# Performance work log

Hardware: AMD Instinct MI355X
Metric: run time of the kernel (lower is better)

Reference implementation:

```python
import jax, jax.numpy as jnp
import numpy as np

N_NODES = 100000
N_EDGES = 1600000


def _tconv(x, src, dst, Wq, bq, Wk, bk, Wv, bv, Ws, bs):
    """PyG TransformerConv (heads=1, concat=True, root_weight=True), eval mode."""
    n = x.shape[0]
    q = x @ Wq + bq          # [N, d]
    k = x @ Wk + bk
    v = x @ Wv + bv
    scale = 1.0 / jnp.sqrt(jnp.asarray(q.shape[1], q.dtype))
    # per-edge attention logits: query at destination, key at source
    alpha = jnp.sum(q[dst] * k[src], axis=-1) * scale       # [E]
    # segment softmax over incoming edges of each destination node
    m = jax.ops.segment_max(alpha, dst, num_segments=n)      # [N]
    e = jnp.exp(alpha - m[dst])
    s = jax.ops.segment_sum(e, dst, num_segments=n)          # [N]
    a = e / s[dst]                                           # [E]
    agg = jax.ops.segment_sum(a[:, None] * v[src], dst, num_segments=n)  # [N, d]
    return agg + x @ Ws + bs  # skip connection (root_weight=True)


def setup_inputs() -> dict:
    key = jax.random.key(0)
    ks = jax.random.split(key, 20)
    x = jax.random.normal(ks[0], (N_NODES, 2), dtype=jnp.float32)
    edge_index = jax.random.randint(ks[1], (2, N_EDGES), 0, N_NODES, dtype=jnp.int64)
    def lin(k, din, dout):
        k1, k2 = jax.random.split(k)
        lim = 1.0 / np.sqrt(din)
        W = jax.random.uniform(k1, (din, dout), jnp.float32, -lim, lim)
        b = jax.random.uniform(k2, (dout,), jnp.float32, -lim, lim)
        return W, b
    Wq1, bq1 = lin(ks[2], 2, 256)
    Wk1, bk1 = lin(ks[3], 2, 256)
    Wv1, bv1 = lin(ks[4], 2, 256)
    Ws1, bs1 = lin(ks[5], 2, 256)
    Wq2, bq2 = lin(ks[6], 256, 2)
    Wk2, bk2 = lin(ks[7], 256, 2)
    Wv2, bv2 = lin(ks[8], 256, 2)
    Ws2, bs2 = lin(ks[9], 256, 2)
    return dict(x=x, edge_index=edge_index,
                Wq1=Wq1, bq1=bq1, Wk1=Wk1, bk1=bk1, Wv1=Wv1, bv1=bv1, Ws1=Ws1, bs1=bs1,
                Wq2=Wq2, bq2=bq2, Wk2=Wk2, bk2=bk2, Wv2=Wv2, bv2=bv2, Ws2=Ws2, bs2=bs2)


def reference(x, edge_index,
              Wq1, bq1, Wk1, bk1, Wv1, bv1, Ws1, bs1,
              Wq2, bq2, Wk2, bk2, Wv2, bv2, Ws2, bs2):
    src, dst = edge_index[0], edge_index[1]
    h = _tconv(x, src, dst, Wq1, bq1, Wk1, bk1, Wv1, bv1, Ws1, bs1)
    h = jax.nn.relu(h)
    # F.dropout is identity in eval mode
    h = _tconv(h, src, dst, Wq2, bq2, Wk2, bk2, Wv2, bv2, Ws2, bs2)
    return jax.nn.log_softmax(h, axis=1)
```

## Files before the change

kernel.cpp:

```cpp
#include <hip/hip_runtime.h>


#define R_LOG2   7
#define R_DSTS   128
#define BE       4096
#define MAXNB    1024
#define CAPB     2432
#define RSQRT2   0.70710678118654752f

__global__ __launch_bounds__(1024) void scatter1_k(
        const int* __restrict__ src, const int* __restrict__ dst,
        int* __restrict__ cnt, int* __restrict__ recs, int NB, int E) {
    __shared__ int hist[MAXNB];
    __shared__ int lofs[MAXNB];
    __shared__ int gbase[MAXNB];
    __shared__ int stage[BE];
    __shared__ unsigned short sbkt[BE];
    __shared__ int wsum[16];
    int t = threadIdx.x;
    if (t < NB) hist[t] = 0;
    __syncthreads();

    int base = blockIdx.x * BE;
    int nloc = E - base; if (nloc > BE) nloc = BE;
    int nv = nloc >> 2;
    const int4* d4 = (const int4*)(dst + base);
    const int4* s4 = (const int4*)(src + base);

    for (int i = t; i < nv; i += 1024) {
        int4 v = d4[i];
        atomicAdd(&hist[v.x >> R_LOG2], 1);
        atomicAdd(&hist[v.y >> R_LOG2], 1);
        atomicAdd(&hist[v.z >> R_LOG2], 1);
        atomicAdd(&hist[v.w >> R_LOG2], 1);
    }
    for (int i = (nv << 2) + t; i < nloc; i += 1024)
        atomicAdd(&hist[dst[base + i] >> R_LOG2], 1);
    __syncthreads();

    {
        int v = (t < NB) ? hist[t] : 0;
        int lane = t & 63, w = t >> 6;
        int incl = v;
#pragma unroll
        for (int o = 1; o < 64; o <<= 1) {
            int u = __shfl_up(incl, o);
            if (lane >= o) incl += u;
        }
        if (lane == 63) wsum[w] = incl;
        __syncthreads();
        int ex = incl - v;
        for (int j = 0; j < w; ++j) ex += wsum[j];
        if (t < NB) lofs[t] = ex;
    }
    __syncthreads();

    if (t < NB) {
        int h = hist[t];
        int start = h ? atomicAdd(&cnt[t], h) : 0;
        gbase[t] = t * CAPB + start - lofs[t];
        hist[t] = 0;
    }
    __syncthreads();

    for (int i = t; i < nv; i += 1024) {
        int4 dv = d4[i];
        int4 sv = s4[i];
        int d, b, r, p;
        d = dv.x; b = d >> R_LOG2; r = atomicAdd(&hist[b], 1); p = lofs[b] + r;
        stage[p] = sv.x | ((d & (R_DSTS - 1)) << 17); sbkt[p] = (unsigned short)b;
        d = dv.y; b = d >> R_LOG2; r = atomicAdd(&hist[b], 1); p = lofs[b] + r;
        stage[p] = sv.y | ((d & (R_DSTS - 1)) << 17); sbkt[p] = (unsigned short)b;
        d = dv.z; b = d >> R_LOG2; r = atomicAdd(&hist[b], 1); p = lofs[b] + r;
        stage[p] = sv.z | ((d & (R_DSTS - 1)) << 17); sbkt[p] = (unsigned short)b;
        d = dv.w; b = d >> R_LOG2; r = atomicAdd(&hist[b], 1); p = lofs[b] + r;
        stage[p] = sv.w | ((d & (R_DSTS - 1)) << 17); sbkt[p] = (unsigned short)b;
    }
    for (int i = (nv << 2) + t; i < nloc; i += 1024) {
        int d = dst[base + i];
        int b = d >> R_LOG2;
        int r = atomicAdd(&hist[b], 1);
        int p = lofs[b] + r;
        stage[p] = src[base + i] | ((d & (R_DSTS - 1)) << 17);
        sbkt[p] = (unsigned short)b;
    }
    __syncthreads();

    for (int i = t; i < nloc; i += 1024) {
        int bk = sbkt[i];
        int p = gbase[bk] + i;
        if (p < (bk + 1) * CAPB) recs[p] = stage[i];
    }
}

__global__ __launch_bounds__(512) void l1agg_k(
        const float* __restrict__ x,
        const float* __restrict__ Wq1, const float* __restrict__ bq1,
        const float* __restrict__ Wk1, const float* __restrict__ bk1,
        const int* __restrict__ recs, const int* __restrict__ cnt,
        float4* __restrict__ agg1, int N) {
    __shared__ float cpart[4][9];
    __shared__ float c9[9];
    __shared__ float p0[R_DSTS], p1[R_DSTS], pc[R_DSTS];
    __shared__ float ac[3 * R_DSTS];
    int t = threadIdx.x;

    if (t < 256) {
        float wq0 = Wq1[t], wq1 = Wq1[256 + t];
        float wk0 = Wk1[t], wk1 = Wk1[256 + t];
        float bq = bq1[t], bk = bk1[t];
        float vals[9] = { wq0 * wk0, wq0 * wk1, wq1 * wk0, wq1 * wk1,
                          wq0 * bk,  wq1 * bk,  bq * wk0,  bq * wk1,  bq * bk };
        int lane = t & 63, w = t >> 6;
#pragma unroll
        for (int i = 0; i < 9; ++i) {
            float v = vals[i];
#pragma unroll
            for (int o = 32; o > 0; o >>= 1) v += __shfl_xor(v, o);
            if (lane == 0) cpart[w][i] = v;
        }
    }
    __syncthreads();
    if (t < 9) c9[t] = cpart[0][t] + cpart[1][t] + cpart[2][t] + cpart[3][t];
    __syncthreads();

    int b = blockIdx.x;
    int nbase = b << R_LOG2;
    int rem = N - nbase; if (rem > R_DSTS) rem = R_DSTS;

    if (t < 3 * R_DSTS) ac[t] = 0.f;
    if (t < rem) {
        float2 xd = ((const float2*)x)[nbase + t];
        p0[t] = c9[0] * xd.x + c9[2] * xd.y + c9[6];
        p1[t] = c9[1] * xd.x + c9[3] * xd.y + c9[7];
        pc[t] = c9[4] * xd.x + c9[5] * xd.y + c9[8];
    }
    __syncthreads();

    int cb = cnt[b]; if (cb > CAPB) cb = CAPB;
    const int* rb = recs + (size_t)b * CAPB;
    for (int i = t; i < cb; i += 512) {
        int rec = rb[i];
        int s = rec & 0x1FFFF;
        int dl = (rec >> 17) & (R_DSTS - 1);
        float2 xs = ((const float2*)x)[s];
        float w = __expf((p0[dl] * xs.x + p1[dl] * xs.y + pc[dl]) * 0.0625f);
        atomicAdd(&ac[dl], w);
        atomicAdd(&ac[R_DSTS + dl], w * xs.x);
        atomicAdd(&ac[2 * R_DSTS + dl], w * xs.y);
    }
    __syncthreads();

    if (t < rem)
        agg1[nbase + t] = make_float4(ac[t], ac[R_DSTS + t], ac[2 * R_DSTS + t], 0.f);
}

__global__ __launch_bounds__(256, 4) void proj_k(
        const float* __restrict__ x, const float4* __restrict__ agg1,
        const float* __restrict__ Wv1, const float* __restrict__ bv1,
        const float* __restrict__ Ws1, const float* __restrict__ bs1,
        const float* __restrict__ Wq2, const float* __restrict__ bq2,
        const float* __restrict__ Wk2, const float* __restrict__ bk2,
        const float* __restrict__ Wv2, const float* __restrict__ bv2,
        const float* __restrict__ Ws2, const float* __restrict__ bs2,
        float* __restrict__ q2, float4* __restrict__ kv2,
        float* __restrict__ hs2, int N) {
    __shared__ float sW[14][256];
    int t = threadIdx.x;
    sW[0][t]  = Wv1[t];
    sW[1][t]  = Wv1[256 + t];
    sW[2][t]  = Ws1[t];
    sW[3][t]  = Ws1[256 + t];
    sW[4][t]  = bv1[t];
    sW[5][t]  = bs1[t];
    sW[6][t]  = Wq2[2 * t];
    sW[7][t]  = Wq2[2 * t + 1];
    sW[8][t]  = Wk2[2 * t];
    sW[9][t]  = Wk2[2 * t + 1];
    sW[10][t] = Wv2[2 * t];
    sW[11][t] = Wv2[2 * t + 1];
    sW[12][t] = Ws2[2 * t];
    sW[13][t] = Ws2[2 * t + 1];
    __syncthreads();

    int g = t & 7;
    int grp = t >> 3;
    int nb = blockIdx.x * 64 + grp * 2;

    float a0[2], a1[2], he[2], xdx[2], xdy[2];
#pragma unroll
    for (int k = 0; k < 2; ++k) {
        int n = nb + k;
        a0[k] = 0.f; a1[k] = 0.f; he[k] = 0.f; xdx[k] = 0.f; xdy[k] = 0.f;
        if (n < N) {
            float4 ag = agg1[n];
            if (ag.x > 0.f) {
                float inv = 1.0f / ag.x;
                a0[k] = ag.y * inv; a1[k] = ag.z * inv; he[k] = 1.f;
            }
            float2 xd = ((const float2*)x)[n];
            xdx[k] = xd.x; xdy[k] = xd.y;
        }
    }

    float acc[2][8];
#pragma unroll
    for (int k = 0; k < 2; ++k)
#pragma unroll
        for (int i = 0; i < 8; ++i) acc[k][i] = 0.f;

#pragma unroll 1
    for (int j = 0; j < 8; ++j) {
        int ci = g + 8 * j;
        float4 hk[2];
        {
            float4 w0 = ((const float4*)sW[0])[ci];
            float4 w1 = ((const float4*)sW[1])[ci];
            float4 w2 = ((const float4*)sW[2])[ci];
            float4 w3 = ((const float4*)sW[3])[ci];
            float4 w4 = ((const float4*)sW[4])[ci];
            float4 w5 = ((const float4*)sW[5])[ci];
#pragma unroll
            for (int k = 0; k < 2; ++k) {
                hk[k].x = fmaxf(a0[k]*w0.x + a1[k]*w1.x + xdx[k]*w2.x + xdy[k]*w3.x + he[k]*w4.x + w5.x, 0.f);
                hk[k].y = fmaxf(a0[k]*w0.y + a1[k]*w1.y + xdx[k]*w2.y + xdy[k]*w3.y + he[k]*w4.y + w5.y, 0.f);
                hk[k].z = fmaxf(a0[k]*w0.z + a1[k]*w1.z + xdx[k]*w2.z + xdy[k]*w3.z + he[k]*w4.z + w5.z, 0.f);
                hk[k].w = fmaxf(a0[k]*w0.w + a1[k]*w1.w + xdx[k]*w2.w + xdy[k]*w3.w + he[k]*w4.w + w5.w, 0.f);
            }
        }
#pragma unroll
        for (int i = 0; i < 8; ++i) {
            float4 u = ((const float4*)sW[6 + i])[ci];
#pragma unroll
            for (int k = 0; k < 2; ++k)
                acc[k][i] += hk[k].x*u.x + hk[k].y*u.y + hk[k].z*u.z + hk[k].w*u.w;
        }
    }
#pragma unroll
    for (int k = 0; k < 2; ++k)
#pragma unroll
        for (int i = 0; i < 8; ++i) {
#pragma unroll
            for (int m = 1; m < 8; m <<= 1)
                acc[k][i] += __shfl_xor(acc[k][i], m);
        }
    if (g < 2) {
        int n = nb + g;
        if (n < N) {
            ((float2*)q2)[n]  = make_float2(acc[g][0] + bq2[0], acc[g][1] + bq2[1]);
            kv2[n] = make_float4(acc[g][2] + bk2[0], acc[g][3] + bk2[1],
                                 acc[g][4] + bv2[0], acc[g][5] + bv2[1]);
            ((float2*)hs2)[n] = make_float2(acc[g][6] + bs2[0], acc[g][7] + bs2[1]);
        }
    }
}

__global__ __launch_bounds__(512) void l2out_k(
        const float* __restrict__ q2, const float4* __restrict__ kv2,
        const float* __restrict__ hs2,
        const int* __restrict__ recs, const int* __restrict__ cnt,
        float* __restrict__ out, int N) {
    __shared__ float qx[R_DSTS], qy[R_DSTS];
    __shared__ float ac[3 * R_DSTS];
    int t = threadIdx.x;
    int b = blockIdx.x;
    int nbase = b << R_LOG2;
    int rem = N - nbase; if (rem > R_DSTS) rem = R_DSTS;

    if (t < 3 * R_DSTS) ac[t] = 0.f;
    if (t < rem) {
        float2 q = ((const float2*)q2)[nbase + t];
        qx[t] = q.x * RSQRT2;
        qy[t] = q.y * RSQRT2;
    }
    __syncthreads();

    int cb = cnt[b]; if (cb > CAPB) cb = CAPB;
    const int* rb = recs + (size_t)b * CAPB;
    for (int i = t; i < cb; i += 512) {
        int rec = rb[i];
        int s = rec & 0x1FFFF;
        int dl = (rec >> 17) & (R_DSTS - 1);
        float4 kv = kv2[s];
        float w = __expf(qx[dl] * kv.x + qy[dl] * kv.y);
        atomicAdd(&ac[dl], w);
        atomicAdd(&ac[R_DSTS + dl], w * kv.z);
        atomicAdd(&ac[2 * R_DSTS + dl], w * kv.w);
    }
    __syncthreads();

    if (t < rem) {
        int n = nbase + t;
        float s = ac[t];
        float g0 = 0.f, g1 = 0.f;
        if (s > 0.f) {
            float inv = 1.0f / s;
            g0 = ac[R_DSTS + t] * inv; g1 = ac[2 * R_DSTS + t] * inv;
        }
        float2 hs = ((const float2*)hs2)[n];
        float o0 = g0 + hs.x;
        float o1 = g1 + hs.y;
        float mx = fmaxf(o0, o1), mn = fminf(o0, o1);
        float lse = mx + log1pf(__expf(mn - mx));
        ((float2*)out)[n] = make_float2(o0 - lse, o1 - lse);
    }
}

extern "C" void kernel_launch(void* const* d_in, const int* in_sizes, int n_in,
                              void* d_out, int out_size, void* d_ws, size_t ws_size,
                              hipStream_t stream) {
    const float* x   = (const float*)d_in[0];
    const int*   ei  = (const int*)d_in[1];
    const float* Wq1 = (const float*)d_in[2];
    const float* bq1 = (const float*)d_in[3];
    const float* Wk1 = (const float*)d_in[4];
    const float* bk1 = (const float*)d_in[5];
    const float* Wv1 = (const float*)d_in[6];
    const float* bv1 = (const float*)d_in[7];
    const float* Ws1 = (const float*)d_in[8];
    const float* bs1 = (const float*)d_in[9];
    const float* Wq2 = (const float*)d_in[10];
    const float* bq2 = (const float*)d_in[11];
    const float* Wk2 = (const float*)d_in[12];
    const float* bk2 = (const float*)d_in[13];
    const float* Wv2 = (const float*)d_in[14];
    const float* bv2 = (const float*)d_in[15];
    const float* Ws2 = (const float*)d_in[16];
    const float* bs2 = (const float*)d_in[17];

    const int N = in_sizes[0] / 2;
    const int E = in_sizes[1] / 2;
    const int* src = ei;
    const int* dst = ei + E;

    const int NB   = (N + R_DSTS - 1) >> R_LOG2;
    const int NBlk = (E + BE - 1) / BE;

    float* ws = (float*)d_ws;
    size_t off = 0;
    int*   cnt   = (int*)(ws + off);         off += NB;
    int*   recs  = (int*)(ws + off);         off += (size_t)NB * CAPB;
    off = (off + 3) & ~(size_t)3;
    float4* agg1 = (float4*)(ws + off);      off += 4 * (size_t)N;
    float4* kv2  = (float4*)(ws + off);      off += 4 * (size_t)N;
    float* q2    = ws + off;                 off += 2 * (size_t)N;
    float* hs2   = ws + off;                 off += 2 * (size_t)N;

    const int gP = (N + 63) / 64;

    hipMemsetAsync(cnt, 0, NB * sizeof(int), stream);
    scatter1_k<<<NBlk, 1024, 0, stream>>>(src, dst, cnt, recs, NB, E);
    l1agg_k<<<NB, 512, 0, stream>>>(x, Wq1, bq1, Wk1, bk1, recs, cnt, agg1, N);
    proj_k<<<gP, 256, 0, stream>>>(x, agg1, Wv1, bv1, Ws1, bs1,
                                   Wq2, bq2, Wk2, bk2, Wv2, bv2, Ws2, bs2,
                                   q2, kv2, hs2, N);
    l2out_k<<<NB, 512, 0, stream>>>(q2, kv2, hs2, recs, cnt, (float*)d_out, N);
}
```

Baseline: 123.3 us.

## Fuse layer-1 aggregation with projection kernel and vectorize edge record loads

Merges the layer-1 attention aggregation kernel with the dense projection kernel, so each 128-destination block projects its own nodes directly from shared-memory accumulators. This removes the agg1 round trip through global memory and one kernel launch. It also reads edge records as int4 in both aggregation loops, so four gathers are in flight per thread. In exchange the fused kernel uses more shared memory (about 14 KB of weights) and runs the projection with 512 threads covering 128 nodes, which may reduce occupancy.

```diff
diff --git a/kernel.cpp b/kernel.cpp
--- a/kernel.cpp
+++ b/kernel.cpp
@@ -93,16 +93,24 @@
     }
 }
 
-__global__ __launch_bounds__(512) void l1agg_k(
+__global__ __launch_bounds__(512) void l1proj_k(
         const float* __restrict__ x,
         const float* __restrict__ Wq1, const float* __restrict__ bq1,
         const float* __restrict__ Wk1, const float* __restrict__ bk1,
+        const float* __restrict__ Wv1, const float* __restrict__ bv1,
+        const float* __restrict__ Ws1, const float* __restrict__ bs1,
+        const float* __restrict__ Wq2, const float* __restrict__ bq2,
+        const float* __restrict__ Wk2, const float* __restrict__ bk2,
+        const float* __restrict__ Wv2, const float* __restrict__ bv2,
+        const float* __restrict__ Ws2, const float* __restrict__ bs2,
         const int* __restrict__ recs, const int* __restrict__ cnt,
-        float4* __restrict__ agg1, int N) {
+        float* __restrict__ q2, float4* __restrict__ kv2,
+        float* __restrict__ hs2, int N) {
     __shared__ float cpart[4][9];
     __shared__ float c9[9];
     __shared__ float p0[R_DSTS], p1[R_DSTS], pc[R_DSTS];
     __shared__ float ac[3 * R_DSTS];
+    __shared__ float sW[14][256];
     int t = threadIdx.x;
 
     if (t < 256) {
@@ -119,8 +127,26 @@
             for (int o = 32; o > 0; o >>= 1) v += __shfl_xor(v, o);
             if (lane == 0) cpart[w][i] = v;
         }
-    }
-    __syncthreads();
+    } else if (t < 512) {
+        int c = t - 256;
+        sW[0][c]  = Wv1[c];
+        sW[1][c]  = Wv1[256 + c];
+        sW[2][c]  = Ws1[c];
+        sW[3][c]  = Ws1[256 + c];
+        sW[4][c]  = bv1[c];
+        sW[5][c]  = bs1[c];
+        sW[6][c]  = Wq2[2 * c];
+        sW[7][c]  = Wq2[2 * c + 1];
+        sW[8][c]  = Wk2[2 * c];
+        sW[9][c]  = Wk2[2 * c + 1];
+        sW[10][c] = Wv2[2 * c];
+        sW[11][c] = Wv2[2 * c + 1];
+        sW[12][c] = Ws2[2 * c];
+        sW[13][c] = Ws2[2 * c + 1];
+    }
+    __syncthreads();
+    if (t < 256) {
+    }
     if (t < 9) c9[t] = cpart[0][t] + cpart[1][t] + cpart[2][t] + cpart[3][t];
     __syncthreads();
 
@@ -137,13 +163,35 @@
     }
     __syncthreads();
 
+    const float2* x2 = (const float2*)x;
     int cb = cnt[b]; if (cb > CAPB) cb = CAPB;
     const int* rb = recs + (size_t)b * CAPB;
-    for (int i = t; i < cb; i += 512) {
+    const int4* rb4 = (const int4*)rb;
+    int nv4 = cb >> 2;
+    for (int i = t; i < nv4; i += 512) {
+        int4 r = rb4[i];
+        int s0 = r.x & 0x1FFFF, d0 = (r.x >> 17) & (R_DSTS - 1);
+        int s1 = r.y & 0x1FFFF, d1 = (r.y >> 17) & (R_DSTS - 1);
+        int s2 = r.z & 0x1FFFF, d2 = (r.z >> 17) & (R_DSTS - 1);
+        int s3 = r.w & 0x1FFFF, d3 = (r.w >> 17) & (R_DSTS - 1);
+        float2 xa = x2[s0];
+        float2 xb = x2[s1];
+        float2 xc = x2[s2];
+        float2 xd = x2[s3];
+        float w0 = __expf((p0[d0] * xa.x + p1[d0] * xa.y + pc[d0]) * 0.0625f);
+        float w1 = __expf((p0[d1] * xb.x + p1[d1] * xb.y + pc[d1]) * 0.0625f);
+        float w2 = __expf((p0[d2] * xc.x + p1[d2] * xc.y + pc[d2]) * 0.0625f);
+        float w3 = __expf((p0[d3] * xd.x + p1[d3] * xd.y + pc[d3]) * 0.0625f);
+        atomicAdd(&ac[d0], w0); atomicAdd(&ac[R_DSTS + d0], w0 * xa.x); atomicAdd(&ac[2 * R_DSTS + d0], w0 * xa.y);
+        atomicAdd(&ac[d1], w1); atomicAdd(&ac[R_DSTS + d1], w1 * xb.x); atomicAdd(&ac[2 * R_DSTS + d1], w1 * xb.y);
+        atomicAdd(&ac[d2], w2); atomicAdd(&ac[R_DSTS + d2], w2 * xc.x); atomicAdd(&ac[2 * R_DSTS + d2], w2 * xc.y);
+        atomicAdd(&ac[d3], w3); atomicAdd(&ac[R_DSTS + d3], w3 * xd.x); atomicAdd(&ac[2 * R_DSTS + d3], w3 * xd.y);
+    }
+    for (int i = (nv4 << 2) + t; i < cb; i += 512) {
         int rec = rb[i];
         int s = rec & 0x1FFFF;
         int dl = (rec >> 17) & (R_DSTS - 1);
-        float2 xs = ((const float2*)x)[s];
+        float2 xs = x2[s];
         float w = __expf((p0[dl] * xs.x + p1[dl] * xs.y + pc[dl]) * 0.0625f);
         atomicAdd(&ac[dl], w);
         atomicAdd(&ac[R_DSTS + dl], w * xs.x);
@@ -151,52 +199,23 @@
     }
     __syncthreads();
 
-    if (t < rem)
-        agg1[nbase + t] = make_float4(ac[t], ac[R_DSTS + t], ac[2 * R_DSTS + t], 0.f);
-}
-
-__global__ __launch_bounds__(256, 4) void proj_k(
-        const float* __restrict__ x, const float4* __restrict__ agg1,
-        const float* __restrict__ Wv1, const float* __restrict__ bv1,
-        const float* __restrict__ Ws1, const float* __restrict__ bs1,
-        const float* __restrict__ Wq2, const float* __restrict__ bq2,
-        const float* __restrict__ Wk2, const float* __restrict__ bk2,
-        const float* __restrict__ Wv2, const float* __restrict__ bv2,
-        const float* __restrict__ Ws2, const float* __restrict__ bs2,
-        float* __restrict__ q2, float4* __restrict__ kv2,
-        float* __restrict__ hs2, int N) {
-    __shared__ float sW[14][256];
-    int t = threadIdx.x;
-    sW[0][t]  = Wv1[t];
-    sW[1][t]  = Wv1[256 + t];
-    sW[2][t]  = Ws1[t];
-    sW[3][t]  = Ws1[256 + t];
-    sW[4][t]  = bv1[t];
-    sW[5][t]  = bs1[t];
-    sW[6][t]  = Wq2[2 * t];
-    sW[7][t]  = Wq2[2 * t + 1];
-    sW[8][t]  = Wk2[2 * t];
-    sW[9][t]  = Wk2[2 * t + 1];
-    sW[10][t] = Wv2[2 * t];
-    sW[11][t] = Wv2[2 * t + 1];
-    sW[12][t] = Ws2[2 * t];
-    sW[13][t] = Ws2[2 * t + 1];
-    __syncthreads();
-
     int g = t & 7;
     int grp = t >> 3;
-    int nb = blockIdx.x * 64 + grp * 2;
+    int i0 = grp * 2;
 
     float a0[2], a1[2], he[2], xdx[2], xdy[2];
 #pragma unroll
     for (int k = 0; k < 2; ++k) {
-        int n = nb + k;
+        int idx = i0 + k;
+        int n = nbase + idx;
         a0[k] = 0.f; a1[k] = 0.f; he[k] = 0.f; xdx[k] = 0.f; xdy[k] = 0.f;
-        if (n < N) {
-            float4 ag = agg1[n];
-            if (ag.x > 0.f) {
-                float inv = 1.0f / ag.x;
-                a0[k] = ag.y * inv; a1[k] = ag.z * inv; he[k] = 1.f;
+        if (idx < rem) {
+            float s = ac[idx];
+            if (s > 0.f) {
+                float inv = 1.0f / s;
+                a0[k] = ac[R_DSTS + idx] * inv;
+                a1[k] = ac[2 * R_DSTS + idx] * inv;
+                he[k] = 1.f;
             }
             float2 xd = ((const float2*)x)[n];
             xdx[k] = xd.x; xdy[k] = xd.y;
@@ -245,8 +264,9 @@
                 acc[k][i] += __shfl_xor(acc[k][i], m);
         }
     if (g < 2) {
-        int n = nb + g;
-        if (n < N) {
+        int idx = i0 + g;
+        int n = nbase + idx;
+        if (idx < rem) {
             ((float2*)q2)[n]  = make_float2(acc[g][0] + bq2[0], acc[g][1] + bq2[1]);
             kv2[n] = make_float4(acc[g][2] + bk2[0], acc[g][3] + bk2[1],
                                  acc[g][4] + bv2[0], acc[g][5] + bv2[1]);
@@ -277,7 +297,28 @@
 
     int cb = cnt[b]; if (cb > CAPB) cb = CAPB;
     const int* rb = recs + (size_t)b * CAPB;
-    for (int i = t; i < cb; i += 512) {
+    const int4* rb4 = (const int4*)rb;
+    int nv4 = cb >> 2;
+    for (int i = t; i < nv4; i += 512) {
+        int4 r = rb4[i];
+        int s0 = r.x & 0x1FFFF, d0 = (r.x >> 17) & (R_DSTS - 1);
+        int s1 = r.y & 0x1FFFF, d1 = (r.y >> 17) & (R_DSTS - 1);
+        int s2 = r.z & 0x1FFFF, d2 = (r.z >> 17) & (R_DSTS - 1);
+        int s3 = r.w & 0x1FFFF, d3 = (r.w >> 17) & (R_DSTS - 1);
+        float4 ka = kv2[s0];
+        float4 kb = kv2[s1];
+        float4 kc = kv2[s2];
+        float4 kd = kv2[s3];
+        float w0 = __expf(qx[d0] * ka.x + qy[d0] * ka.y);
+        float w1 = __expf(qx[d1] * kb.x + qy[d1] * kb.y);
+        float w2 = __expf(qx[d2] * kc.x + qy[d2] * kc.y);
+        float w3 = __expf(qx[d3] * kd.x + qy[d3] * kd.y);
+        atomicAdd(&ac[d0], w0); atomicAdd(&ac[R_DSTS + d0], w0 * ka.z); atomicAdd(&ac[2 * R_DSTS + d0], w0 * ka.w);
+        atomicAdd(&ac[d1], w1); atomicAdd(&ac[R_DSTS + d1], w1 * kb.z); atomicAdd(&ac[2 * R_DSTS + d1], w1 * kb.w);
+        atomicAdd(&ac[d2], w2); atomicAdd(&ac[R_DSTS + d2], w2 * kc.z); atomicAdd(&ac[2 * R_DSTS + d2], w2 * kc.w);
+        atomicAdd(&ac[d3], w3); atomicAdd(&ac[R_DSTS + d3], w3 * kd.z); atomicAdd(&ac[2 * R_DSTS + d3], w3 * kd.w);
+    }
+    for (int i = (nv4 << 2) + t; i < cb; i += 512) {
         int rec = rb[i];
         int s = rec & 0x1FFFF;
         int dl = (rec >> 17) & (R_DSTS - 1);
@@ -338,21 +379,18 @@
 
     float* ws = (float*)d_ws;
     size_t off = 0;
-    int*   cnt   = (int*)(ws + off);         off += NB;
-    int*   recs  = (int*)(ws + off);         off += (size_t)NB * CAPB;
+    int*   cnt  = (int*)(ws + off);      off += MAXNB;
+    int*   recs = (int*)(ws + off);      off += (size_t)NB * CAPB;
     off = (off + 3) & ~(size_t)3;
-    float4* agg1 = (float4*)(ws + off);      off += 4 * (size_t)N;
-    float4* kv2  = (float4*)(ws + off);      off += 4 * (size_t)N;
-    float* q2    = ws + off;                 off += 2 * (size_t)N;
-    float* hs2   = ws + off;                 off += 2 * (size_t)N;
-
-    const int gP = (N + 63) / 64;
+    float4* kv2 = (float4*)(ws + off);   off += 4 * (size_t)N;
+    float* q2   = ws + off;              off += 2 * (size_t)N;
+    float* hs2  = ws + off;              off += 2 * (size_t)N;
 
     hipMemsetAsync(cnt, 0, NB * sizeof(int), stream);
     scatter1_k<<<NBlk, 1024, 0, stream>>>(src, dst, cnt, recs, NB, E);
-    l1agg_k<<<NB, 512, 0, stream>>>(x, Wq1, bq1, Wk1, bk1, recs, cnt, agg1, N);
-    proj_k<<<gP, 256, 0, stream>>>(x, agg1, Wv1, bv1, Ws1, bs1,
-                                   Wq2, bq2, Wk2, bk2, Wv2, bv2, Ws2, bs2,
-                                   q2, kv2, hs2, N);
+    l1proj_k<<<NB, 512, 0, stream>>>(x, Wq1, bq1, Wk1, bk1,
+                                     Wv1, bv1, Ws1, bs1,
+                                     Wq2, bq2, Wk2, bk2, Wv2, bv2, Ws2, bs2,
+                                     recs, cnt, q2, kv2, hs2, N);
     l2out_k<<<NB, 512, 0, stream>>>(q2, kv2, hs2, recs, cnt, (float*)d_out, N);
 }
```

Measured after the change: 120.6 us. 1.02x faster.
